# Kernel optimization log

Measured on AMD Instinct MI355X. Metric: run time of the kernel, lower is better.

Reference implementation:

```python
import jax, jax.numpy as jnp
import numpy as np

WT, WX = 101, 11
SIGMA_TAU, SIGMA_HX = 21.0, 11.0
EPS = 1e-9


def _gauss1d(n, sigma):
    xx = jnp.arange(n, dtype=jnp.float32) - n // 2
    k = jnp.exp(-(xx ** 2) / (2.0 * sigma ** 2))
    return k / k.sum()


def _smooth(img, k_t, k_x):
    # img: [B, 1, T, X]; separable Gaussian window (exact: 2D kernel is outer product)
    dn = ('NCHW', 'OIHW', 'NCHW')
    out = jax.lax.conv_general_dilated(img, k_t.reshape(1, 1, -1, 1), (1, 1), 'SAME', dimension_numbers=dn)
    out = jax.lax.conv_general_dilated(out, k_x.reshape(1, 1, 1, -1), (1, 1), 'SAME', dimension_numbers=dn)
    return out


def setup_inputs() -> dict:
    key = jax.random.key(0)
    kx, ky = jax.random.split(key)
    shape = (16, 1, 2500, 512)
    return {
        'x': jax.random.normal(kx, shape, dtype=jnp.float32),
        'y': jax.random.normal(ky, shape, dtype=jnp.float32),
    }


def reference(x, y):
    k_t = _gauss1d(WT, SIGMA_TAU)
    k_x = _gauss1d(WX, SIGMA_HX)
    mu_x = _smooth(x, k_t, k_x)
    mu_y = _smooth(y, k_t, k_x)
    var_x = _smooth(x * x, k_t, k_x) - mu_x * mu_x
    var_y = _smooth(y * y, k_t, k_x) - mu_y * mu_y
    cov_xy = _smooth(x * y, k_t, k_x) - mu_x * mu_y
    # normalized local coherence map in [-1, 1]
    cs = cov_xy * jax.lax.rsqrt(var_x * var_y + EPS)
    return (1.0 - cs).mean()
```

## Files before the change

kernel.cpp:

```cpp
#include <hip/hip_runtime.h>
#include <hip/hip_bf16.h>

#define B_   16
#define T_   2500
#define X_   512
#define XT   32
#define SEGS 4
#define SEGR 640
#define NSX  (X_ / XT)
#define NBLK (B_ * SEGS * NSX)

typedef __attribute__((ext_vector_type(4))) float f32x4;

__device__ __forceinline__ void barrier_lgkm() {
    asm volatile("s_waitcnt lgkmcnt(0)\n\ts_barrier" ::: "memory");
}

__global__ __launch_bounds__(256, 4) void coh9(const float* __restrict__ xg,
                                               const float* __restrict__ yg,
                                               float* __restrict__ partial)
{
    __shared__ float ktn[104];
    __shared__ float kxn[12];
    __shared__ float norm2[2];
    __shared__ unsigned long long XS[18][5][34];
    __shared__ unsigned long long PBq[2][5][16][9];
    __shared__ float wred[4];

    const int tid  = threadIdx.x;
    const int lane = tid & 63;
    const int w    = tid >> 6;
    const int g    = lane >> 4;
    const int ln16 = lane & 15;
    const int pair = w >> 1;
    const int p01  = w & 1;

    const int bid = blockIdx.x;
    const int wid = (bid & 7) * (NBLK / 8) + (bid >> 3);
    const int xt  = wid & 15;
    const int seg = (wid >> 4) & 3;
    const int b   = wid >> 6;

    const int x0    = xt * XT;
    const int t0    = seg * SEGR;
    const int t_end = min(t0 + SEGR, T_);
    const int nm    = (t_end - t0 + 15) >> 4;
    const int itmax = nm + 8;

    if (tid < 104) ktn[tid] = 0.0f;
    if (tid < 12)  kxn[tid] = 0.0f;
    __syncthreads();
    if (tid < 101) { float d = (float)(tid - 50); ktn[tid] = expf(-d * d / (2.0f * 21.0f * 21.0f)); }
    if (tid < 11)  { float d = (float)(tid - 5);  kxn[tid] = expf(-d * d / (2.0f * 11.0f * 11.0f)); }
    __syncthreads();
    if (tid == 0) {
        float s = 0.f; for (int i = 0; i < 101; ++i) s += ktn[i]; norm2[0] = 1.0f / s;
        s = 0.f;       for (int i = 0; i < 11;  ++i) s += kxn[i]; norm2[1] = 1.0f / s;
    }
    __syncthreads();
    if (tid < 101) ktn[tid] *= norm2[0];
    if (tid < 11)  kxn[tid] *= norm2[1];
    __syncthreads();

    const float* xb = xg + (size_t)b * T_ * X_;
    const float* yb = yg + (size_t)b * T_ * X_;

    float local = 0.f;

    if (pair == 0) {
        long a_x;
        {
            float vv[8];
#pragma unroll
            for (int sl = 0; sl < 8; ++sl) {
                int idx = 8 * g + sl - ln16 - 3;
                vv[sl] = (idx >= 0 && idx <= 10) ? kxn[idx] * 16.0f : 0.0f;
            }
            int lo = __builtin_amdgcn_cvt_pk_fp8_f32(vv[0], vv[1], 0, false);
            lo     = __builtin_amdgcn_cvt_pk_fp8_f32(vv[2], vv[3], lo, true);
            int hi = __builtin_amdgcn_cvt_pk_fp8_f32(vv[4], vv[5], 0, false);
            hi     = __builtin_amdgcn_cvt_pk_fp8_f32(vv[6], vv[7], hi, true);
            a_x = (long)(((unsigned long long)(unsigned)hi << 32) | (unsigned)lo);
        }
        const uint sel1  = (ln16 & 1) ? 0x07030602u : 0x01050004u;
        const uint sel2  = (ln16 & 2) ? 0x07060302u : 0x01000504u;
        const int  cidx  = ((ln16 & 1) << 1) | ((ln16 >> 1) & 1);
        const int  abyte = (ln16 & 4);
        const int  uhalf = (ln16 >> 3);

        const int  gcol  = x0 - 16 + 4 * ln16;
        const bool colOK = (gcol >= 0) && (gcol < X_);

        float4 xv[2], yv[2];
#pragma unroll
        for (int s = 0; s < 2; ++s) {
            int grow = t0 - 56 + 8 * p01 + 4 * s + g;
            bool ok = colOK && (grow >= 0) && (grow < T_);
            xv[s] = ok ? *(const float4*)(xb + (size_t)grow * X_ + gcol) : make_float4(0.f, 0.f, 0.f, 0.f);
            yv[s] = ok ? *(const float4*)(yb + (size_t)grow * X_ + gcol) : make_float4(0.f, 0.f, 0.f, 0.f);
        }

        int gbase = 0;
        for (int it = 0; it <= itmax; ++it) {
            if (it >= 1 && it <= nm + 7) {
                int u0 = gbase + 16; if (u0 >= 18) u0 -= 18;
                int u1 = u0 + 1;     if (u1 >= 18) u1 -= 18;
                const int uu = uhalf ? u1 : u0;
                const int sb = (it - 1) & 1;
#pragma unroll
                for (int f = 0; f < 5; ++f) {
                    long bfrag = (long)PBq[sb][f][ln16][1 + 2 * p01 + g];
                    f32x4 z; z[0] = 0.f; z[1] = 0.f; z[2] = 0.f; z[3] = 0.f;
                    f32x4 d = __builtin_amdgcn_mfma_f32_16x16x32_fp8_fp8(a_x, bfrag, z, 0, 0, 0);
                    int pk = __builtin_amdgcn_cvt_pk_fp8_f32(d[0], d[1], 0, false);
                    pk     = __builtin_amdgcn_cvt_pk_fp8_f32(d[2], d[3], pk, true);
                    uint pkc   = (uint)pk;
                    uint part1 = (uint)__builtin_amdgcn_update_dpp(0, (int)pkc, 177, 0xF, 0xF, true);
                    uint s1v   = __builtin_amdgcn_perm(pkc, part1, sel1);
                    uint part2 = (uint)__builtin_amdgcn_update_dpp(0, (int)s1v, 78, 0xF, 0xF, true);
                    uint Tt    = __builtin_amdgcn_perm(s1v, part2, sel2);
                    *(uint*)((uchar*)&XS[uu][f][16 * p01 + 4 * g + cidx] + abyte) = Tt;
                }
            }
            if (it <= nm + 6) {
                const int db = it & 1;
#pragma unroll
                for (int s = 0; s < 2; ++s) {
                    int rrs = 8 * p01 + 4 * s + g;
                    float4 X = xv[s], Y = yv[s];
                    int q0 = __builtin_amdgcn_cvt_pk_fp8_f32(X.x, X.y, 0, false);
                    q0     = __builtin_amdgcn_cvt_pk_fp8_f32(X.z, X.w, q0, true);
                    int q1 = __builtin_amdgcn_cvt_pk_fp8_f32(Y.x, Y.y, 0, false);
                    q1     = __builtin_amdgcn_cvt_pk_fp8_f32(Y.z, Y.w, q1, true);
                    int q2 = __builtin_amdgcn_cvt_pk_fp8_f32(X.x * X.x, X.y * X.y, 0, false);
                    q2     = __builtin_amdgcn_cvt_pk_fp8_f32(X.z * X.z, X.w * X.w, q2, true);
                    int q3 = __builtin_amdgcn_cvt_pk_fp8_f32(Y.x * Y.x, Y.y * Y.y, 0, false);
                    q3     = __builtin_amdgcn_cvt_pk_fp8_f32(Y.z * Y.z, Y.w * Y.w, q3, true);
                    int q4 = __builtin_amdgcn_cvt_pk_fp8_f32(X.x * Y.x, X.y * Y.y, 0, false);
                    q4     = __builtin_amdgcn_cvt_pk_fp8_f32(X.z * Y.z, X.w * Y.w, q4, true);
                    *(uint*)((uchar*)&PBq[db][0][rrs][0] + 4 * ln16) = (uint)q0;
                    *(uint*)((uchar*)&PBq[db][1][rrs][0] + 4 * ln16) = (uint)q1;
                    *(uint*)((uchar*)&PBq[db][2][rrs][0] + 4 * ln16) = (uint)q2;
                    *(uint*)((uchar*)&PBq[db][3][rrs][0] + 4 * ln16) = (uint)q3;
                    *(uint*)((uchar*)&PBq[db][4][rrs][0] + 4 * ln16) = (uint)q4;
                }
            }
            if (it + 1 <= nm + 6) {
#pragma unroll
                for (int s = 0; s < 2; ++s) {
                    int grow = t0 - 56 + 16 * (it + 1) + 8 * p01 + 4 * s + g;
                    bool ok = colOK && (grow >= 0) && (grow < T_);
                    xv[s] = ok ? *(const float4*)(xb + (size_t)grow * X_ + gcol) : make_float4(0.f, 0.f, 0.f, 0.f);
                    yv[s] = ok ? *(const float4*)(yb + (size_t)grow * X_ + gcol) : make_float4(0.f, 0.f, 0.f, 0.f);
                }
            }
            barrier_lgkm();
            gbase += 2; if (gbase >= 18) gbase -= 18;
        }
    } else {
        long a_t[4];
#pragma unroll
        for (int c = 0; c < 4; ++c) {
            float vv[8];
#pragma unroll
            for (int sl = 0; sl < 8; ++sl) {
                int idx = 32 * c + 8 * g + sl - ln16 - 6;
                vv[sl] = (idx >= 0 && idx <= 100) ? ktn[idx] * 16.0f : 0.0f;
            }
            int lo = __builtin_amdgcn_cvt_pk_fp8_f32(vv[0], vv[1], 0, false);
            lo     = __builtin_amdgcn_cvt_pk_fp8_f32(vv[2], vv[3], lo, true);
            int hi = __builtin_amdgcn_cvt_pk_fp8_f32(vv[4], vv[5], 0, false);
            hi     = __builtin_amdgcn_cvt_pk_fp8_f32(vv[6], vv[7], hi, true);
            a_t[c] = (long)(((unsigned long long)(unsigned)hi << 32) | (unsigned)lo);
        }

        int gbase = 0;
        for (int it = 0; it <= itmax; ++it) {
            if (it >= 9) {
                const int m = it - 9;
                f32x4 acc[5];
#pragma unroll
                for (int f = 0; f < 5; ++f) { acc[f][0] = 0.f; acc[f][1] = 0.f; acc[f][2] = 0.f; acc[f][3] = 0.f; }
#pragma unroll
                for (int c = 0; c < 4; ++c) {
                    int u = gbase + 4 * c + g; if (u >= 18) u -= 18;
#pragma unroll
                    for (int f = 0; f < 5; ++f) {
                        long bfrag = (long)XS[u][f][16 * p01 + ln16];
                        acc[f] = __builtin_amdgcn_mfma_f32_16x16x32_fp8_fp8(a_t[c], bfrag, acc[f], 0, 0, 0);
                    }
                }
                const float s_ = 1.0f / 256.0f;
#pragma unroll
                for (int r = 0; r < 4; ++r) {
                    int t = t0 + 16 * m + 4 * g + r;
                    if (t < t_end) {
                        float a0 = acc[0][r], a1 = acc[1][r];
                        float sa0 = a0 * s_, sa1 = a1 * s_;
                        float cov = fmaf(-sa0, a1, acc[4][r]);
                        float vx  = fmaf(-sa0, a0, acc[2][r]);
                        float vy  = fmaf(-sa1, a1, acc[3][r]);
                        local += 1.0f - cov * rsqrtf(fmaf(vx, vy, 6.5536e-5f));
                    }
                }
            }
            barrier_lgkm();
            gbase += 2; if (gbase >= 18) gbase -= 18;
        }
    }

#pragma unroll
    for (int off = 32; off >= 1; off >>= 1) local += __shfl_down(local, off);
    if ((tid & 63) == 0) wred[tid >> 6] = local;
    __syncthreads();
    if (tid == 0)
        partial[wid] = wred[0] + wred[1] + wred[2] + wred[3];
}

__global__ __launch_bounds__(256) void coh_reduce(const float* __restrict__ partial,
                                                  float* __restrict__ out) {
    __shared__ float wred[4];
    const int tid = threadIdx.x;
    float s = 0.0f;
    for (int i = tid; i < NBLK; i += 256) s += partial[i];
#pragma unroll
    for (int off = 32; off >= 1; off >>= 1) s += __shfl_down(s, off);
    if ((tid & 63) == 0) wred[tid >> 6] = s;
    __syncthreads();
    if (tid == 0)
        out[0] = (wred[0] + wred[1] + wred[2] + wred[3]) *
                 (1.0f / ((float)B_ * (float)T_ * (float)X_));
}

extern "C" void kernel_launch(void* const* d_in, const int* in_sizes, int n_in,
                              void* d_out, int out_size, void* d_ws, size_t ws_size,
                              hipStream_t stream) {
    const float* x = (const float*)d_in[0];
    const float* y = (const float*)d_in[1];
    float* out = (float*)d_out;
    float* partial = (float*)d_ws;

    coh9<<<dim3(NBLK), 256, 0, stream>>>(x, y, partial);
    coh_reduce<<<1, 256, 0, stream>>>(partial, out);
}
```

Measured before the change: 61.66 us.

## Restructure pipeline with two barriers per step to shrink LDS and raise occupancy

Replaces the double-buffered PB staging and the 18-slot XS ring with a single PB buffer and a 16-slot ring indexed by a power-of-two mask. Each step now has two barriers: one between the PB write and the x-direction MFMA, and one between the XS write and the t-direction MFMA. The smaller LDS footprint supports launch bounds of 6 blocks per CU instead of 4. Filter weights are now computed in registers with no shared-memory setup or syncthreads, and interior tiles use fast paths without bounds checks. The cost is an extra barrier per iteration and tighter register limits.

```diff
diff --git a/kernel.cpp b/kernel.cpp
--- a/kernel.cpp
+++ b/kernel.cpp
@@ -1,5 +1,4 @@
 #include <hip/hip_runtime.h>
-#include <hip/hip_bf16.h>
 
 #define B_   16
 #define T_   2500
@@ -16,15 +15,12 @@
     asm volatile("s_waitcnt lgkmcnt(0)\n\ts_barrier" ::: "memory");
 }
 
-__global__ __launch_bounds__(256, 4) void coh9(const float* __restrict__ xg,
-                                               const float* __restrict__ yg,
-                                               float* __restrict__ partial)
+__global__ __launch_bounds__(256, 6) void coh10(const float* __restrict__ xg,
+                                                const float* __restrict__ yg,
+                                                float* __restrict__ partial)
 {
-    __shared__ float ktn[104];
-    __shared__ float kxn[12];
-    __shared__ float norm2[2];
-    __shared__ unsigned long long XS[18][5][34];
-    __shared__ unsigned long long PBq[2][5][16][9];
+    __shared__ unsigned long long XS[16][5][32];
+    __shared__ unsigned long long PB[5][16][9];
     __shared__ float wred[4];
 
     const int tid  = threadIdx.x;
@@ -45,22 +41,7 @@
     const int t0    = seg * SEGR;
     const int t_end = min(t0 + SEGR, T_);
     const int nm    = (t_end - t0 + 15) >> 4;
-    const int itmax = nm + 8;
-
-    if (tid < 104) ktn[tid] = 0.0f;
-    if (tid < 12)  kxn[tid] = 0.0f;
-    __syncthreads();
-    if (tid < 101) { float d = (float)(tid - 50); ktn[tid] = expf(-d * d / (2.0f * 21.0f * 21.0f)); }
-    if (tid < 11)  { float d = (float)(tid - 5);  kxn[tid] = expf(-d * d / (2.0f * 11.0f * 11.0f)); }
-    __syncthreads();
-    if (tid == 0) {
-        float s = 0.f; for (int i = 0; i < 101; ++i) s += ktn[i]; norm2[0] = 1.0f / s;
-        s = 0.f;       for (int i = 0; i < 11;  ++i) s += kxn[i]; norm2[1] = 1.0f / s;
-    }
-    __syncthreads();
-    if (tid < 101) ktn[tid] *= norm2[0];
-    if (tid < 11)  kxn[tid] *= norm2[1];
-    __syncthreads();
+    const int pmax  = nm + 7;
 
     const float* xb = xg + (size_t)b * T_ * X_;
     const float* yb = yg + (size_t)b * T_ * X_;
@@ -68,13 +49,19 @@
     float local = 0.f;
 
     if (pair == 0) {
+        float ksum_x = 0.f;
+#pragma unroll 1
+        for (int i = 0; i < 11; ++i) { float d = (float)(i - 5); ksum_x += expf(-d * d * (1.0f / 242.0f)); }
+        const float scx = 16.0f / ksum_x;
         long a_x;
         {
             float vv[8];
 #pragma unroll
             for (int sl = 0; sl < 8; ++sl) {
                 int idx = 8 * g + sl - ln16 - 3;
-                vv[sl] = (idx >= 0 && idx <= 10) ? kxn[idx] * 16.0f : 0.0f;
+                float d = (float)(idx - 5);
+                float v = expf(-d * d * (1.0f / 242.0f)) * scx;
+                vv[sl] = (idx >= 0 && idx <= 10) ? v : 0.0f;
             }
             int lo = __builtin_amdgcn_cvt_pk_fp8_f32(vv[0], vv[1], 0, false);
             lo     = __builtin_amdgcn_cvt_pk_fp8_f32(vv[2], vv[3], lo, true);
@@ -90,40 +77,35 @@
 
         const int  gcol  = x0 - 16 + 4 * ln16;
         const bool colOK = (gcol >= 0) && (gcol < X_);
+        const float* xpl = xb + gcol;
+        const float* ypl = yb + gcol;
+        const float4 z4  = make_float4(0.f, 0.f, 0.f, 0.f);
 
         float4 xv[2], yv[2];
-#pragma unroll
-        for (int s = 0; s < 2; ++s) {
-            int grow = t0 - 56 + 8 * p01 + 4 * s + g;
-            bool ok = colOK && (grow >= 0) && (grow < T_);
-            xv[s] = ok ? *(const float4*)(xb + (size_t)grow * X_ + gcol) : make_float4(0.f, 0.f, 0.f, 0.f);
-            yv[s] = ok ? *(const float4*)(yb + (size_t)grow * X_ + gcol) : make_float4(0.f, 0.f, 0.f, 0.f);
-        }
-
-        int gbase = 0;
-        for (int it = 0; it <= itmax; ++it) {
-            if (it >= 1 && it <= nm + 7) {
-                int u0 = gbase + 16; if (u0 >= 18) u0 -= 18;
-                int u1 = u0 + 1;     if (u1 >= 18) u1 -= 18;
-                const int uu = uhalf ? u1 : u0;
-                const int sb = (it - 1) & 1;
-#pragma unroll
-                for (int f = 0; f < 5; ++f) {
-                    long bfrag = (long)PBq[sb][f][ln16][1 + 2 * p01 + g];
-                    f32x4 z; z[0] = 0.f; z[1] = 0.f; z[2] = 0.f; z[3] = 0.f;
-                    f32x4 d = __builtin_amdgcn_mfma_f32_16x16x32_fp8_fp8(a_x, bfrag, z, 0, 0, 0);
-                    int pk = __builtin_amdgcn_cvt_pk_fp8_f32(d[0], d[1], 0, false);
-                    pk     = __builtin_amdgcn_cvt_pk_fp8_f32(d[2], d[3], pk, true);
-                    uint pkc   = (uint)pk;
-                    uint part1 = (uint)__builtin_amdgcn_update_dpp(0, (int)pkc, 177, 0xF, 0xF, true);
-                    uint s1v   = __builtin_amdgcn_perm(pkc, part1, sel1);
-                    uint part2 = (uint)__builtin_amdgcn_update_dpp(0, (int)s1v, 78, 0xF, 0xF, true);
-                    uint Tt    = __builtin_amdgcn_perm(s1v, part2, sel2);
-                    *(uint*)((uchar*)&XS[uu][f][16 * p01 + 4 * g + cidx] + abyte) = Tt;
-                }
-            }
-            if (it <= nm + 6) {
-                const int db = it & 1;
+        auto issue_loads = [&](int c) {
+            const int rowlo = t0 - 56 + 16 * c;
+            if (rowlo >= 0 && rowlo + 15 < T_) {
+#pragma unroll
+                for (int s = 0; s < 2; ++s) {
+                    int grow = rowlo + 8 * p01 + 4 * s + g;
+                    xv[s] = colOK ? *(const float4*)(xpl + (size_t)grow * X_) : z4;
+                    yv[s] = colOK ? *(const float4*)(ypl + (size_t)grow * X_) : z4;
+                }
+            } else {
+#pragma unroll
+                for (int s = 0; s < 2; ++s) {
+                    int grow = rowlo + 8 * p01 + 4 * s + g;
+                    bool ok = colOK && (grow >= 0) && (grow < T_);
+                    xv[s] = ok ? *(const float4*)(xpl + (size_t)grow * X_) : z4;
+                    yv[s] = ok ? *(const float4*)(ypl + (size_t)grow * X_) : z4;
+                }
+            }
+        };
+        issue_loads(0);
+
+        int gb = 0;
+        for (int p = 0; p <= pmax; ++p) {
+            if (p <= nm + 6) {
 #pragma unroll
                 for (int s = 0; s < 2; ++s) {
                     int rrs = 8 * p01 + 4 * s + g;
@@ -138,26 +120,40 @@
                     q3     = __builtin_amdgcn_cvt_pk_fp8_f32(Y.z * Y.z, Y.w * Y.w, q3, true);
                     int q4 = __builtin_amdgcn_cvt_pk_fp8_f32(X.x * Y.x, X.y * Y.y, 0, false);
                     q4     = __builtin_amdgcn_cvt_pk_fp8_f32(X.z * Y.z, X.w * Y.w, q4, true);
-                    *(uint*)((uchar*)&PBq[db][0][rrs][0] + 4 * ln16) = (uint)q0;
-                    *(uint*)((uchar*)&PBq[db][1][rrs][0] + 4 * ln16) = (uint)q1;
-                    *(uint*)((uchar*)&PBq[db][2][rrs][0] + 4 * ln16) = (uint)q2;
-                    *(uint*)((uchar*)&PBq[db][3][rrs][0] + 4 * ln16) = (uint)q3;
-                    *(uint*)((uchar*)&PBq[db][4][rrs][0] + 4 * ln16) = (uint)q4;
-                }
-            }
-            if (it + 1 <= nm + 6) {
-#pragma unroll
-                for (int s = 0; s < 2; ++s) {
-                    int grow = t0 - 56 + 16 * (it + 1) + 8 * p01 + 4 * s + g;
-                    bool ok = colOK && (grow >= 0) && (grow < T_);
-                    xv[s] = ok ? *(const float4*)(xb + (size_t)grow * X_ + gcol) : make_float4(0.f, 0.f, 0.f, 0.f);
-                    yv[s] = ok ? *(const float4*)(yb + (size_t)grow * X_ + gcol) : make_float4(0.f, 0.f, 0.f, 0.f);
-                }
-            }
-            barrier_lgkm();
-            gbase += 2; if (gbase >= 18) gbase -= 18;
+                    *(uint*)((uchar*)&PB[0][rrs][0] + 4 * ln16) = (uint)q0;
+                    *(uint*)((uchar*)&PB[1][rrs][0] + 4 * ln16) = (uint)q1;
+                    *(uint*)((uchar*)&PB[2][rrs][0] + 4 * ln16) = (uint)q2;
+                    *(uint*)((uchar*)&PB[3][rrs][0] + 4 * ln16) = (uint)q3;
+                    *(uint*)((uchar*)&PB[4][rrs][0] + 4 * ln16) = (uint)q4;
+                }
+            }
+            if (p + 1 <= nm + 6) issue_loads(p + 1);
+            barrier_lgkm();
+            if (p <= nm + 6) {
+                const int uu = (gb + uhalf) & 15;
+#pragma unroll
+                for (int f = 0; f < 5; ++f) {
+                    long bfrag = (long)PB[f][ln16][1 + 2 * p01 + g];
+                    f32x4 z; z[0] = 0.f; z[1] = 0.f; z[2] = 0.f; z[3] = 0.f;
+                    f32x4 d = __builtin_amdgcn_mfma_f32_16x16x32_fp8_fp8(a_x, bfrag, z, 0, 0, 0);
+                    int pk = __builtin_amdgcn_cvt_pk_fp8_f32(d[0], d[1], 0, false);
+                    pk     = __builtin_amdgcn_cvt_pk_fp8_f32(d[2], d[3], pk, true);
+                    uint pkc   = (uint)pk;
+                    uint part1 = (uint)__builtin_amdgcn_update_dpp(0, (int)pkc, 177, 0xF, 0xF, true);
+                    uint s1v   = __builtin_amdgcn_perm(pkc, part1, sel1);
+                    uint part2 = (uint)__builtin_amdgcn_update_dpp(0, (int)s1v, 78, 0xF, 0xF, true);
+                    uint Tt    = __builtin_amdgcn_perm(s1v, part2, sel2);
+                    *(uint*)((uchar*)&XS[uu][f][16 * p01 + 4 * g + cidx] + abyte) = Tt;
+                }
+            }
+            barrier_lgkm();
+            gb = (gb + 2) & 15;
         }
     } else {
+        float ksum_t = 0.f;
+#pragma unroll 1
+        for (int i = 0; i < 101; ++i) { float d = (float)(i - 50); ksum_t += expf(-d * d * (1.0f / 882.0f)); }
+        const float sct = 16.0f / ksum_t;
         long a_t[4];
 #pragma unroll
         for (int c = 0; c < 4; ++c) {
@@ -165,7 +161,9 @@
 #pragma unroll
             for (int sl = 0; sl < 8; ++sl) {
                 int idx = 32 * c + 8 * g + sl - ln16 - 6;
-                vv[sl] = (idx >= 0 && idx <= 100) ? ktn[idx] * 16.0f : 0.0f;
+                float d = (float)(idx - 50);
+                float v = expf(-d * d * (1.0f / 882.0f)) * sct;
+                vv[sl] = (idx >= 0 && idx <= 100) ? v : 0.0f;
             }
             int lo = __builtin_amdgcn_cvt_pk_fp8_f32(vv[0], vv[1], 0, false);
             lo     = __builtin_amdgcn_cvt_pk_fp8_f32(vv[2], vv[3], lo, true);
@@ -174,27 +172,29 @@
             a_t[c] = (long)(((unsigned long long)(unsigned)hi << 32) | (unsigned)lo);
         }
 
-        int gbase = 0;
-        for (int it = 0; it <= itmax; ++it) {
-            if (it >= 9) {
-                const int m = it - 9;
-                f32x4 acc[5];
+        int gb = 0;
+        for (int p = 0; p <= pmax; ++p) {
+            f32x4 acc[5];
+            if (p >= 8) {
 #pragma unroll
                 for (int f = 0; f < 5; ++f) { acc[f][0] = 0.f; acc[f][1] = 0.f; acc[f][2] = 0.f; acc[f][3] = 0.f; }
 #pragma unroll
                 for (int c = 0; c < 4; ++c) {
-                    int u = gbase + 4 * c + g; if (u >= 18) u -= 18;
+                    int u = (gb + 4 * c + g) & 15;
 #pragma unroll
                     for (int f = 0; f < 5; ++f) {
                         long bfrag = (long)XS[u][f][16 * p01 + ln16];
                         acc[f] = __builtin_amdgcn_mfma_f32_16x16x32_fp8_fp8(a_t[c], bfrag, acc[f], 0, 0, 0);
                     }
                 }
+            }
+            barrier_lgkm();
+            if (p >= 8) {
+                const int m = p - 8;
                 const float s_ = 1.0f / 256.0f;
-#pragma unroll
-                for (int r = 0; r < 4; ++r) {
-                    int t = t0 + 16 * m + 4 * g + r;
-                    if (t < t_end) {
+                if (16 * m + 15 < t_end - t0) {
+#pragma unroll
+                    for (int r = 0; r < 4; ++r) {
                         float a0 = acc[0][r], a1 = acc[1][r];
                         float sa0 = a0 * s_, sa1 = a1 * s_;
                         float cov = fmaf(-sa0, a1, acc[4][r]);
@@ -202,10 +202,23 @@
                         float vy  = fmaf(-sa1, a1, acc[3][r]);
                         local += 1.0f - cov * rsqrtf(fmaf(vx, vy, 6.5536e-5f));
                     }
-                }
-            }
-            barrier_lgkm();
-            gbase += 2; if (gbase >= 18) gbase -= 18;
+                } else {
+#pragma unroll
+                    for (int r = 0; r < 4; ++r) {
+                        int t = t0 + 16 * m + 4 * g + r;
+                        if (t < t_end) {
+                            float a0 = acc[0][r], a1 = acc[1][r];
+                            float sa0 = a0 * s_, sa1 = a1 * s_;
+                            float cov = fmaf(-sa0, a1, acc[4][r]);
+                            float vx  = fmaf(-sa0, a0, acc[2][r]);
+                            float vy  = fmaf(-sa1, a1, acc[3][r]);
+                            local += 1.0f - cov * rsqrtf(fmaf(vx, vy, 6.5536e-5f));
+                        }
+                    }
+                }
+            }
+            barrier_lgkm();
+            gb = (gb + 2) & 15;
         }
     }
 
@@ -240,6 +253,6 @@
     float* out = (float*)d_out;
     float* partial = (float*)d_ws;
 
-    coh9<<<dim3(NBLK), 256, 0, stream>>>(x, y, partial);
+    coh10<<<dim3(NBLK), 256, 0, stream>>>(x, y, partial);
     coh_reduce<<<1, 256, 0, stream>>>(partial, out);
 }
```

Measured after the change: 93.98 us. 1.52x slower.

## Enlarge XS ring to add a pipeline stage and hoist B-fragment loads

Applied to the files above, without the earlier changes.

The intermediate XS ring buffer grows from 18 to 20 slots and the consumer starts one iteration later, adding slack between the x-pass producer writes and the t-pass consumer reads. The consumer waves now load all 20 B fragments from LDS before issuing the MFMA chain, so the LDS reads are not interleaved with the dependent MFMAs. The wave-pair role assignment is also alternated per block via XOR with the block id, which changes which SIMDs run producer versus consumer work. This costs more LDS and registers per block and adds one more loop iteration of pipeline latency.

```diff
diff --git a/kernel.cpp b/kernel.cpp
--- a/kernel.cpp
+++ b/kernel.cpp
@@ -1,5 +1,4 @@
 #include <hip/hip_runtime.h>
-#include <hip/hip_bf16.h>
 
 #define B_   16
 #define T_   2500
@@ -9,6 +8,7 @@
 #define SEGR 640
 #define NSX  (X_ / XT)
 #define NBLK (B_ * SEGS * NSX)
+#define RING 20
 
 typedef __attribute__((ext_vector_type(4))) float f32x4;
 
@@ -16,14 +16,14 @@
     asm volatile("s_waitcnt lgkmcnt(0)\n\ts_barrier" ::: "memory");
 }
 
-__global__ __launch_bounds__(256, 4) void coh9(const float* __restrict__ xg,
-                                               const float* __restrict__ yg,
-                                               float* __restrict__ partial)
+__global__ __launch_bounds__(256, 4) void coh11(const float* __restrict__ xg,
+                                                const float* __restrict__ yg,
+                                                float* __restrict__ partial)
 {
     __shared__ float ktn[104];
     __shared__ float kxn[12];
     __shared__ float norm2[2];
-    __shared__ unsigned long long XS[18][5][34];
+    __shared__ unsigned long long XS[RING][5][34];
     __shared__ unsigned long long PBq[2][5][16][9];
     __shared__ float wred[4];
 
@@ -32,7 +32,6 @@
     const int w    = tid >> 6;
     const int g    = lane >> 4;
     const int ln16 = lane & 15;
-    const int pair = w >> 1;
     const int p01  = w & 1;
 
     const int bid = blockIdx.x;
@@ -41,11 +40,13 @@
     const int seg = (wid >> 4) & 3;
     const int b   = wid >> 6;
 
+    const int pair = ((w >> 1) ^ wid) & 1;
+
     const int x0    = xt * XT;
     const int t0    = seg * SEGR;
     const int t_end = min(t0 + SEGR, T_);
     const int nm    = (t_end - t0 + 15) >> 4;
-    const int itmax = nm + 8;
+    const int pmax  = nm + 9;
 
     if (tid < 104) ktn[tid] = 0.0f;
     if (tid < 12)  kxn[tid] = 0.0f;
@@ -100,12 +101,11 @@
             yv[s] = ok ? *(const float4*)(yb + (size_t)grow * X_ + gcol) : make_float4(0.f, 0.f, 0.f, 0.f);
         }
 
-        int gbase = 0;
-        for (int it = 0; it <= itmax; ++it) {
+        int gb = 0;
+        for (int it = 0; it <= pmax; ++it) {
             if (it >= 1 && it <= nm + 7) {
-                int u0 = gbase + 16; if (u0 >= 18) u0 -= 18;
-                int u1 = u0 + 1;     if (u1 >= 18) u1 -= 18;
-                const int uu = uhalf ? u1 : u0;
+                int u0 = gb + 18; if (u0 >= RING) u0 -= RING;
+                const int uu = u0 + uhalf;
                 const int sb = (it - 1) & 1;
 #pragma unroll
                 for (int f = 0; f < 5; ++f) {
@@ -155,7 +155,7 @@
                 }
             }
             barrier_lgkm();
-            gbase += 2; if (gbase >= 18) gbase -= 18;
+            gb += 2; if (gb >= RING) gb -= RING;
         }
     } else {
         long a_t[4];
@@ -174,22 +174,38 @@
             a_t[c] = (long)(((unsigned long long)(unsigned)hi << 32) | (unsigned)lo);
         }
 
-        int gbase = 0;
-        for (int it = 0; it <= itmax; ++it) {
-            if (it >= 9) {
-                const int m = it - 9;
+        int gb = 0;
+        for (int it = 0; it <= pmax; ++it) {
+            if (it >= 10) {
+                const int m = it - 10;
+                long bf0[5], bf1[5], bf2[5], bf3[5];
+                {
+                    int u0 = gb + g;      if (u0 >= RING) u0 -= RING;
+                    int u1 = gb + 4 + g;  if (u1 >= RING) u1 -= RING;
+                    int u2 = gb + 8 + g;  if (u2 >= RING) u2 -= RING;
+                    int u3 = gb + 12 + g; if (u3 >= RING) u3 -= RING;
+                    const int nn = 16 * p01 + ln16;
+#pragma unroll
+                    for (int f = 0; f < 5; ++f) bf0[f] = (long)XS[u0][f][nn];
+#pragma unroll
+                    for (int f = 0; f < 5; ++f) bf1[f] = (long)XS[u1][f][nn];
+#pragma unroll
+                    for (int f = 0; f < 5; ++f) bf2[f] = (long)XS[u2][f][nn];
+#pragma unroll
+                    for (int f = 0; f < 5; ++f) bf3[f] = (long)XS[u3][f][nn];
+                }
                 f32x4 acc[5];
 #pragma unroll
                 for (int f = 0; f < 5; ++f) { acc[f][0] = 0.f; acc[f][1] = 0.f; acc[f][2] = 0.f; acc[f][3] = 0.f; }
 #pragma unroll
-                for (int c = 0; c < 4; ++c) {
-                    int u = gbase + 4 * c + g; if (u >= 18) u -= 18;
-#pragma unroll
-                    for (int f = 0; f < 5; ++f) {
-                        long bfrag = (long)XS[u][f][16 * p01 + ln16];
-                        acc[f] = __builtin_amdgcn_mfma_f32_16x16x32_fp8_fp8(a_t[c], bfrag, acc[f], 0, 0, 0);
-                    }
-                }
+                for (int f = 0; f < 5; ++f) acc[f] = __builtin_amdgcn_mfma_f32_16x16x32_fp8_fp8(a_t[0], bf0[f], acc[f], 0, 0, 0);
+#pragma unroll
+                for (int f = 0; f < 5; ++f) acc[f] = __builtin_amdgcn_mfma_f32_16x16x32_fp8_fp8(a_t[1], bf1[f], acc[f], 0, 0, 0);
+#pragma unroll
+                for (int f = 0; f < 5; ++f) acc[f] = __builtin_amdgcn_mfma_f32_16x16x32_fp8_fp8(a_t[2], bf2[f], acc[f], 0, 0, 0);
+#pragma unroll
+                for (int f = 0; f < 5; ++f) acc[f] = __builtin_amdgcn_mfma_f32_16x16x32_fp8_fp8(a_t[3], bf3[f], acc[f], 0, 0, 0);
+
                 const float s_ = 1.0f / 256.0f;
 #pragma unroll
                 for (int r = 0; r < 4; ++r) {
@@ -205,7 +221,7 @@
                 }
             }
             barrier_lgkm();
-            gbase += 2; if (gbase >= 18) gbase -= 18;
+            gb += 2; if (gb >= RING) gb -= RING;
         }
     }
 
@@ -240,6 +256,6 @@
     float* out = (float*)d_out;
     float* partial = (float*)d_ws;
 
-    coh9<<<dim3(NBLK), 256, 0, stream>>>(x, y, partial);
+    coh11<<<dim3(NBLK), 256, 0, stream>>>(x, y, partial);
     coh_reduce<<<1, 256, 0, stream>>>(partial, out);
 }
```

Measured after the change: 62.01 us. No clear change (+0.6%).
